# Performance work log

Measured on AMD Instinct MI355X. Metric: run time of the kernel, lower is better.

The kernel has to match this reference:

```python
import jax, jax.numpy as jnp
import numpy as np

B, N, M, LDIM, RDIM, AGG = 4, 512, 512, 512, 512, 256


def setup_inputs() -> dict:
    key = jax.random.key(0)
    ks = jax.random.split(key, 7)
    data = jax.random.normal(ks[0], (B, N, LDIM), dtype=jnp.float32)
    crit = jax.random.normal(ks[1], (B, M, RDIM), dtype=jnp.float32)
    Wl = jax.random.normal(ks[2], (LDIM, AGG), dtype=jnp.float32) / np.sqrt(LDIM)
    bl = jax.random.normal(ks[3], (AGG,), dtype=jnp.float32) * 0.01
    Wr = jax.random.normal(ks[4], (RDIM, AGG), dtype=jnp.float32) / np.sqrt(RDIM)
    br = jax.random.normal(ks[5], (AGG,), dtype=jnp.float32) * 0.01
    agg = jax.random.uniform(ks[6], (AGG,), dtype=jnp.float32, minval=-0.01, maxval=0.01)
    return {"data": data, "crit": crit, "Wl": Wl, "bl": bl, "Wr": Wr, "br": br, "agg": agg}


def reference(data, crit, Wl, bl, Wr, br, agg):
    # linear projections
    datalin = jnp.einsum('bnl,la->bna', data, Wl) + bl   # [B,N,A]
    critlin = jnp.einsum('bmr,ra->bma', crit, Wr) + br   # [B,M,A]
    # broadcast add -> tanh -> reduce with agg vector: [B,N,M]
    linsum = jnp.tanh(datalin[:, :, None, :] + critlin[:, None, :, :])  # [B,N,M,A]
    dists = jnp.einsum('bnma,a->bnm', linsum, agg)
    return dists
```

## Files before the change

### kernel.cpp

```cpp
#include <hip/hip_runtime.h>


#define A_DIM 256
#define K_DIM 512
#define NROWS 2048

typedef unsigned short ushort;
typedef __attribute__((ext_vector_type(4))) unsigned short us4;
typedef __attribute__((ext_vector_type(8))) unsigned short us8;
typedef __attribute__((ext_vector_type(8))) short short8;
typedef __attribute__((ext_vector_type(4))) float f32x4;
typedef __attribute__((ext_vector_type(2))) float f32x2;

__device__ inline ushort f2bf(float x) {
    union { float f; unsigned u; } v; v.f = x;
    unsigned r = v.u + 0x7FFFu + ((v.u >> 16) & 1u);
    return (ushort)(r >> 16);
}
__device__ inline float bf2f(ushort h) {
    union { unsigned u; float f; } v; v.u = ((unsigned)h) << 16; return v.f;
}
__device__ inline unsigned pack2bf(float lo, float hi) {
    return (unsigned)f2bf(lo) | ((unsigned)f2bf(hi) << 16);
}
__device__ inline f32x2 fma2(f32x2 a, f32x2 b, f32x2 c) {
    return __builtin_elementwise_fma(a, b, c);
}

__global__ __launch_bounds__(256) void transpose_w_kernel(
    const float* __restrict__ Wl, const float* __restrict__ Wr,
    ushort* __restrict__ wt)
{
    __shared__ float tile[64][68];
    const int t   = threadIdx.x;
    const int bid = blockIdx.x;
    const int at  = bid & 3;
    const int kt  = (bid >> 2) & 7;
    const int src = bid >> 5;
    const int a0 = at * 64, k0 = kt * 64;
    const float* W = src ? Wr : Wl;
    ushort* out = wt + (size_t)src * (A_DIM * K_DIM);

    const int c4 = (t & 15) * 4;
    const int kr = t >> 4;
#pragma unroll
    for (int r = 0; r < 4; r++) {
        const int k = kr + r * 16;
        *(float4*)&tile[k][c4] = *(const float4*)(W + (size_t)(k0 + k) * A_DIM + a0 + c4);
    }
    __syncthreads();
    const int aL  = t & 63;
    const int ks0 = (t >> 6) * 16;
#pragma unroll
    for (int g = 0; g < 4; g++) {
        us4 o;
#pragma unroll
        for (int i = 0; i < 4; i++) o[i] = f2bf(tile[ks0 + g * 4 + i][aL]);
        __builtin_nontemporal_store(o, (us4*)(out + (size_t)(a0 + aL) * K_DIM + k0 + ks0 + g * 4));
    }
}

__global__ __launch_bounds__(256) void proj_mfma_kernel(
    const float* __restrict__ data, const float* __restrict__ crit,
    const float* __restrict__ bl, const float* __restrict__ br,
    const ushort* __restrict__ wt, ushort* __restrict__ eplanes)
{
    __shared__ ushort Ws[64][264];

    const int t   = threadIdx.x;
    const int bid = blockIdx.x;
    const int ct  = bid & 3;
    const int rt  = bid >> 2;
    const int src = rt >> 6;
    const int lr0 = (rt & 63) * 32;
    const int c0  = ct * 64;

    const float* X    = src ? crit : data;
    const float* bias = src ? br : bl;
    const ushort* Wt  = wt + (size_t)src * (A_DIM * K_DIM);
    ushort* E = eplanes + (size_t)src * ((size_t)A_DIM * NROWS);

    const int lane = t & 63;
    const int wid  = t >> 6;
    const int wm   = wid >> 1, wn = wid & 1;
    const int quad = lane >> 4, l16 = lane & 15;

    const float* xrow = X + (size_t)(lr0 + wm * 16 + l16) * K_DIM + quad * 8;
    const int aloc0 = wn * 32 + l16;

    f32x4 acc0 = {0.f, 0.f, 0.f, 0.f}, acc1 = {0.f, 0.f, 0.f, 0.f};

    float4 pa = *(const float4*)(xrow);
    float4 pb = *(const float4*)(xrow + 4);

    for (int kc = 0; kc < 2; kc++) {
        __syncthreads();
        {
            const int a  = t & 63;
            const int ks = (t >> 6) * 64;
            const ushort* s = Wt + (size_t)(c0 + a) * K_DIM + kc * 256 + ks;
#pragma unroll
            for (int i = 0; i < 8; i++)
                *(us8*)&Ws[a][ks + i * 8] = *(const us8*)(s + i * 8);
        }
        __syncthreads();

#pragma unroll
        for (int ls = 0; ls < 8; ls++) {
            const int s = kc * 8 + ls;
            float4 ca = pa, cb = pb;
            if (s < 15) {
                pa = *(const float4*)(xrow + (s + 1) * 32);
                pb = *(const float4*)(xrow + (s + 1) * 32 + 4);
            }
            union { short8 s8; unsigned u[4]; } af;
            af.u[0] = pack2bf(ca.x, ca.y);
            af.u[1] = pack2bf(ca.z, ca.w);
            af.u[2] = pack2bf(cb.x, cb.y);
            af.u[3] = pack2bf(cb.z, cb.w);
            short8 b0 = *(const short8*)&Ws[aloc0     ][ls * 32 + quad * 8];
            short8 b1 = *(const short8*)&Ws[aloc0 + 16][ls * 32 + quad * 8];
            acc0 = __builtin_amdgcn_mfma_f32_16x16x32_bf16(af.s8, b0, acc0, 0, 0, 0);
            acc1 = __builtin_amdgcn_mfma_f32_16x16x32_bf16(af.s8, b1, acc1, 0, 0, 0);
        }
    }

    const float c2 = 2.8853900817779268f;
    const int a_col0 = c0 + wn * 32 + l16;
    const int a_col1 = a_col0 + 16;
    const int row0   = lr0 + wm * 16 + quad * 4;
    const float bv0 = bias[a_col0], bv1 = bias[a_col1];
    us4 e0, e1;
#pragma unroll
    for (int i = 0; i < 4; i++) {
        float v0 = (acc0[i] + bv0) * c2;
        float v1 = (acc1[i] + bv1) * c2;
        v0 = fminf(fmaxf(v0, -15.f), 15.f);
        v1 = fminf(fmaxf(v1, -15.f), 15.f);
        e0[i] = f2bf(__builtin_amdgcn_exp2f(v0));
        e1[i] = f2bf(__builtin_amdgcn_exp2f(v1));
    }
    __builtin_nontemporal_store(e0, (us4*)(E + (size_t)a_col0 * NROWS + row0));
    __builtin_nontemporal_store(e1, (us4*)(E + (size_t)a_col1 * NROWS + row0));
}

__global__ __launch_bounds__(512) void tanh_reduce_kernel(
    const ushort* __restrict__ eplanes, const float* __restrict__ agg,
    float* __restrict__ out)
{
    __shared__ __align__(16) float et [2][64][68];
    __shared__ __align__(16) float ect[2][64][68];
    __shared__ __align__(16) float aggs[256];

    const int t  = threadIdx.x;
    const int h  = t >> 8;
    const int u  = t & 255;
    const int m0 = blockIdx.x * 64;
    const int n0 = blockIdx.y * 64;
    const int b  = blockIdx.z;

    const size_t PLANE = (size_t)A_DIM * NROWS;
    const ushort* Ed = eplanes;
    const ushort* Ec = eplanes + PLANE;
    const int row_n = b * 512 + n0;
    const int row_m = b * 512 + m0;

    const int tx = u & 15;
    const int ty = u >> 4;

    if (t < 256) aggs[t] = 2.0f * agg[t];

    f32x2 acc2[4][2];
#pragma unroll
    for (int i = 0; i < 4; i++) { acc2[i][0] = (f32x2)0.f; acc2[i][1] = (f32x2)0.f; }
    float sagg = 0.f;

    const int aL = u >> 2;
    const int qd = u & 3;

    float (*eth)[68]  = et[h];
    float (*ecth)[68] = ect[h];

    us4 pn[4], pm[4];
#pragma unroll
    for (int r = 0; r < 4; r++) {
        const size_t base = (size_t)(h * 128 + aL) * NROWS;
        pn[r] = *(const us4*)(Ed + base + row_n + qd * 16 + r * 4);
        pm[r] = *(const us4*)(Ec + base + row_m + qd * 16 + r * 4);
    }

    for (int ch = 0; ch < 2; ch++) {
        __syncthreads();
#pragma unroll
        for (int r = 0; r < 4; r++) {
            float4 ev, cv;
            ev.x = bf2f(pn[r][0]); ev.y = bf2f(pn[r][1]);
            ev.z = bf2f(pn[r][2]); ev.w = bf2f(pn[r][3]);
            cv.x = bf2f(pm[r][0]); cv.y = bf2f(pm[r][1]);
            cv.z = bf2f(pm[r][2]); cv.w = bf2f(pm[r][3]);
            *(float4*)&eth [aL][qd * 16 + r * 4] = ev;
            *(float4*)&ecth[aL][qd * 16 + r * 4] = cv;
        }
        __syncthreads();
        if (ch == 0) {
            const size_t base = (size_t)(h * 128 + 64 + aL) * NROWS;
#pragma unroll
            for (int r = 0; r < 4; r++) {
                pn[r] = *(const us4*)(Ed + base + row_n + qd * 16 + r * 4);
                pm[r] = *(const us4*)(Ec + base + row_m + qd * 16 + r * 4);
            }
        }

        for (int qg = 0; qg < 16; qg++) {
            const float4 ag = *(const float4*)&aggs[h * 128 + ch * 64 + qg * 4];
            sagg += (ag.x + ag.y) + (ag.z + ag.w);
            float  en[4][4];
            f32x2  fm[4][2];
#pragma unroll
            for (int v = 0; v < 4; v++) {
                float4 e4 = *(const float4*)&eth [qg * 4 + v][ty * 4];
                float4 f4 = *(const float4*)&ecth[qg * 4 + v][tx * 4];
                en[v][0] = e4.x; en[v][1] = e4.y; en[v][2] = e4.z; en[v][3] = e4.w;
                fm[v][0] = f32x2{f4.x, f4.y};
                fm[v][1] = f32x2{f4.z, f4.w};
            }
#pragma unroll
            for (int i = 0; i < 4; i++)
#pragma unroll
                for (int jp = 0; jp < 2; jp++) {
                    const f32x2 one = (f32x2)1.f;
                    f32x2 q0 = fma2((f32x2)en[0][i], fm[0][jp], one);
                    f32x2 q1 = fma2((f32x2)en[1][i], fm[1][jp], one);
                    f32x2 q2 = fma2((f32x2)en[2][i], fm[2][jp], one);
                    f32x2 q3 = fma2((f32x2)en[3][i], fm[3][jp], one);
                    f32x2 q01 = q0 * q1, q23 = q2 * q3;
                    f32x2 n01 = fma2((f32x2)ag.x, q1, (f32x2)ag.y * q0);
                    f32x2 n23 = fma2((f32x2)ag.z, q3, (f32x2)ag.w * q2);
                    f32x2 N   = fma2(n01, q23, n23 * q01);
                    f32x2 D   = q01 * q23;
                    f32x2 r;
                    r.x = __builtin_amdgcn_rcpf(D.x);
                    r.y = __builtin_amdgcn_rcpf(D.y);
                    acc2[i][jp] = fma2(N, r, acc2[i][jp]);
                }
        }
    }

    const float base = 0.5f * sagg;
    float* xb = (float*)ect;
    __syncthreads();
    if (h == 1) {
#pragma unroll
        for (int i = 0; i < 4; i++)
#pragma unroll
            for (int jp = 0; jp < 2; jp++) {
                xb[u * 17 + i * 4 + jp * 2 + 0] = base - acc2[i][jp].x;
                xb[u * 17 + i * 4 + jp * 2 + 1] = base - acc2[i][jp].y;
            }
    }
    __syncthreads();
    if (h == 0) {
#pragma unroll
        for (int i = 0; i < 4; i++) {
            f32x4 v;
            v.x = (base - acc2[i][0].x) + xb[u * 17 + i * 4 + 0];
            v.y = (base - acc2[i][0].y) + xb[u * 17 + i * 4 + 1];
            v.z = (base - acc2[i][1].x) + xb[u * 17 + i * 4 + 2];
            v.w = (base - acc2[i][1].y) + xb[u * 17 + i * 4 + 3];
            __builtin_nontemporal_store(v,
                (f32x4*)(out + ((size_t)(b * 512 + n0 + ty * 4 + i) * 512) + m0 + tx * 4));
        }
    }
}

extern "C" void kernel_launch(void* const* d_in, const int* in_sizes, int n_in,
                              void* d_out, int out_size, void* d_ws, size_t ws_size,
                              hipStream_t stream) {
    const float* data = (const float*)d_in[0];
    const float* crit = (const float*)d_in[1];
    const float* Wl   = (const float*)d_in[2];
    const float* bl   = (const float*)d_in[3];
    const float* Wr   = (const float*)d_in[4];
    const float* br   = (const float*)d_in[5];
    const float* agg  = (const float*)d_in[6];
    float* out = (float*)d_out;

    ushort* eplanes = (ushort*)d_ws;
    ushort* wt      = eplanes + 2 * (size_t)A_DIM * NROWS;

    transpose_w_kernel<<<dim3(64), 256, 0, stream>>>(Wl, Wr, wt);

    proj_mfma_kernel<<<dim3(512), 256, 0, stream>>>(data, crit, bl, br, wt, eplanes);

    tanh_reduce_kernel<<<dim3(8, 8, 4), 512, 0, stream>>>(eplanes, agg, out);
}
```

Baseline: 107.8 us.

## Split tanh reduction across four thread groups and single-stage projection weight load

The tanh-reduce kernel now runs 1024 threads per block, with four groups each owning a 64-wide slice of the aggregation dimension. This removes the two-chunk sequential loop, and the four partial results are combined through shared memory. The projection kernel loads the whole 512-wide weight slice into LDS in one stage, prefetches inputs two steps ahead, and reorders block indices so that blocks sharing a weight column tile launch together. The costs are more LDS per block (about 140KB in the reduce kernel), fewer resident blocks per CU, and a larger cross-group reduction at the end.

```diff
diff --git a/kernel.cpp b/kernel.cpp
--- a/kernel.cpp
+++ b/kernel.cpp
@@ -65,12 +65,12 @@
     const float* __restrict__ bl, const float* __restrict__ br,
     const ushort* __restrict__ wt, ushort* __restrict__ eplanes)
 {
-    __shared__ ushort Ws[64][264];
+    __shared__ ushort Ws[64][520];
 
     const int t   = threadIdx.x;
     const int bid = blockIdx.x;
-    const int ct  = bid & 3;
-    const int rt  = bid >> 2;
+    const int ct  = bid >> 7;
+    const int rt  = bid & 127;
     const int src = rt >> 6;
     const int lr0 = (rt & 63) * 32;
     const int c0  = ct * 64;
@@ -90,39 +90,39 @@
 
     f32x4 acc0 = {0.f, 0.f, 0.f, 0.f}, acc1 = {0.f, 0.f, 0.f, 0.f};
 
-    float4 pa = *(const float4*)(xrow);
-    float4 pb = *(const float4*)(xrow + 4);
-
-    for (int kc = 0; kc < 2; kc++) {
-        __syncthreads();
-        {
-            const int a  = t & 63;
-            const int ks = (t >> 6) * 64;
-            const ushort* s = Wt + (size_t)(c0 + a) * K_DIM + kc * 256 + ks;
-#pragma unroll
-            for (int i = 0; i < 8; i++)
-                *(us8*)&Ws[a][ks + i * 8] = *(const us8*)(s + i * 8);
-        }
-        __syncthreads();
-
-#pragma unroll
-        for (int ls = 0; ls < 8; ls++) {
-            const int s = kc * 8 + ls;
-            float4 ca = pa, cb = pb;
-            if (s < 15) {
-                pa = *(const float4*)(xrow + (s + 1) * 32);
-                pb = *(const float4*)(xrow + (s + 1) * 32 + 4);
-            }
-            union { short8 s8; unsigned u[4]; } af;
-            af.u[0] = pack2bf(ca.x, ca.y);
-            af.u[1] = pack2bf(ca.z, ca.w);
-            af.u[2] = pack2bf(cb.x, cb.y);
-            af.u[3] = pack2bf(cb.z, cb.w);
-            short8 b0 = *(const short8*)&Ws[aloc0     ][ls * 32 + quad * 8];
-            short8 b1 = *(const short8*)&Ws[aloc0 + 16][ls * 32 + quad * 8];
-            acc0 = __builtin_amdgcn_mfma_f32_16x16x32_bf16(af.s8, b0, acc0, 0, 0, 0);
-            acc1 = __builtin_amdgcn_mfma_f32_16x16x32_bf16(af.s8, b1, acc1, 0, 0, 0);
-        }
+    {
+        const int a  = t & 63;
+        const int ks = (t >> 6) * 128;
+        const ushort* s = Wt + (size_t)(c0 + a) * K_DIM + ks;
+#pragma unroll
+        for (int i = 0; i < 16; i++)
+            *(us8*)&Ws[a][ks + i * 8] = *(const us8*)(s + i * 8);
+    }
+
+    float4 pa0 = *(const float4*)(xrow);
+    float4 pb0 = *(const float4*)(xrow + 4);
+    float4 pa1 = *(const float4*)(xrow + 32);
+    float4 pb1 = *(const float4*)(xrow + 36);
+
+    __syncthreads();
+
+#pragma unroll
+    for (int s = 0; s < 16; s++) {
+        float4 ca = pa0, cb = pb0;
+        pa0 = pa1; pb0 = pb1;
+        if (s < 14) {
+            pa1 = *(const float4*)(xrow + (s + 2) * 32);
+            pb1 = *(const float4*)(xrow + (s + 2) * 32 + 4);
+        }
+        union { short8 s8; unsigned u[4]; } af;
+        af.u[0] = pack2bf(ca.x, ca.y);
+        af.u[1] = pack2bf(ca.z, ca.w);
+        af.u[2] = pack2bf(cb.x, cb.y);
+        af.u[3] = pack2bf(cb.z, cb.w);
+        short8 b0 = *(const short8*)&Ws[aloc0     ][s * 32 + quad * 8];
+        short8 b1 = *(const short8*)&Ws[aloc0 + 16][s * 32 + quad * 8];
+        acc0 = __builtin_amdgcn_mfma_f32_16x16x32_bf16(af.s8, b0, acc0, 0, 0, 0);
+        acc1 = __builtin_amdgcn_mfma_f32_16x16x32_bf16(af.s8, b1, acc1, 0, 0, 0);
     }
 
     const float c2 = 2.8853900817779268f;
@@ -144,12 +144,12 @@
     __builtin_nontemporal_store(e1, (us4*)(E + (size_t)a_col1 * NROWS + row0));
 }
 
-__global__ __launch_bounds__(512) void tanh_reduce_kernel(
+__global__ __launch_bounds__(1024) void tanh_reduce_kernel(
     const ushort* __restrict__ eplanes, const float* __restrict__ agg,
     float* __restrict__ out)
 {
-    __shared__ __align__(16) float et [2][64][68];
-    __shared__ __align__(16) float ect[2][64][68];
+    __shared__ __align__(16) float et [4][64][68];
+    __shared__ __align__(16) float ect[4][64][68];
     __shared__ __align__(16) float aggs[256];
 
     const int t  = threadIdx.x;
@@ -181,16 +181,14 @@
     float (*eth)[68]  = et[h];
     float (*ecth)[68] = ect[h];
 
-    us4 pn[4], pm[4];
-#pragma unroll
-    for (int r = 0; r < 4; r++) {
-        const size_t base = (size_t)(h * 128 + aL) * NROWS;
-        pn[r] = *(const us4*)(Ed + base + row_n + qd * 16 + r * 4);
-        pm[r] = *(const us4*)(Ec + base + row_m + qd * 16 + r * 4);
-    }
-
-    for (int ch = 0; ch < 2; ch++) {
-        __syncthreads();
+    {
+        const size_t base = (size_t)(h * 64 + aL) * NROWS;
+        us4 pn[4], pm[4];
+#pragma unroll
+        for (int r = 0; r < 4; r++) {
+            pn[r] = *(const us4*)(Ed + base + row_n + qd * 16 + r * 4);
+            pm[r] = *(const us4*)(Ec + base + row_m + qd * 16 + r * 4);
+        }
 #pragma unroll
         for (int r = 0; r < 4; r++) {
             float4 ev, cv;
@@ -201,72 +199,68 @@
             *(float4*)&eth [aL][qd * 16 + r * 4] = ev;
             *(float4*)&ecth[aL][qd * 16 + r * 4] = cv;
         }
-        __syncthreads();
-        if (ch == 0) {
-            const size_t base = (size_t)(h * 128 + 64 + aL) * NROWS;
-#pragma unroll
-            for (int r = 0; r < 4; r++) {
-                pn[r] = *(const us4*)(Ed + base + row_n + qd * 16 + r * 4);
-                pm[r] = *(const us4*)(Ec + base + row_m + qd * 16 + r * 4);
+    }
+    __syncthreads();
+
+    for (int qg = 0; qg < 16; qg++) {
+        const float4 ag = *(const float4*)&aggs[h * 64 + qg * 4];
+        sagg += (ag.x + ag.y) + (ag.z + ag.w);
+        float  en[4][4];
+        f32x2  fm[4][2];
+#pragma unroll
+        for (int v = 0; v < 4; v++) {
+            float4 e4 = *(const float4*)&eth [qg * 4 + v][ty * 4];
+            float4 f4 = *(const float4*)&ecth[qg * 4 + v][tx * 4];
+            en[v][0] = e4.x; en[v][1] = e4.y; en[v][2] = e4.z; en[v][3] = e4.w;
+            fm[v][0] = f32x2{f4.x, f4.y};
+            fm[v][1] = f32x2{f4.z, f4.w};
+        }
+#pragma unroll
+        for (int i = 0; i < 4; i++)
+#pragma unroll
+            for (int jp = 0; jp < 2; jp++) {
+                const f32x2 one = (f32x2)1.f;
+                f32x2 q0 = fma2((f32x2)en[0][i], fm[0][jp], one);
+                f32x2 q1 = fma2((f32x2)en[1][i], fm[1][jp], one);
+                f32x2 q2 = fma2((f32x2)en[2][i], fm[2][jp], one);
+                f32x2 q3 = fma2((f32x2)en[3][i], fm[3][jp], one);
+                f32x2 q01 = q0 * q1, q23 = q2 * q3;
+                f32x2 n01 = fma2((f32x2)ag.x, q1, (f32x2)ag.y * q0);
+                f32x2 n23 = fma2((f32x2)ag.z, q3, (f32x2)ag.w * q2);
+                f32x2 N   = fma2(n01, q23, n23 * q01);
+                f32x2 D   = q01 * q23;
+                f32x2 r;
+                r.x = __builtin_amdgcn_rcpf(D.x);
+                r.y = __builtin_amdgcn_rcpf(D.y);
+                acc2[i][jp] = fma2(N, r, acc2[i][jp]);
             }
-        }
-
-        for (int qg = 0; qg < 16; qg++) {
-            const float4 ag = *(const float4*)&aggs[h * 128 + ch * 64 + qg * 4];
-            sagg += (ag.x + ag.y) + (ag.z + ag.w);
-            float  en[4][4];
-            f32x2  fm[4][2];
-#pragma unroll
-            for (int v = 0; v < 4; v++) {
-                float4 e4 = *(const float4*)&eth [qg * 4 + v][ty * 4];
-                float4 f4 = *(const float4*)&ecth[qg * 4 + v][tx * 4];
-                en[v][0] = e4.x; en[v][1] = e4.y; en[v][2] = e4.z; en[v][3] = e4.w;
-                fm[v][0] = f32x2{f4.x, f4.y};
-                fm[v][1] = f32x2{f4.z, f4.w};
-            }
-#pragma unroll
-            for (int i = 0; i < 4; i++)
-#pragma unroll
-                for (int jp = 0; jp < 2; jp++) {
-                    const f32x2 one = (f32x2)1.f;
-                    f32x2 q0 = fma2((f32x2)en[0][i], fm[0][jp], one);
-                    f32x2 q1 = fma2((f32x2)en[1][i], fm[1][jp], one);
-                    f32x2 q2 = fma2((f32x2)en[2][i], fm[2][jp], one);
-                    f32x2 q3 = fma2((f32x2)en[3][i], fm[3][jp], one);
-                    f32x2 q01 = q0 * q1, q23 = q2 * q3;
-                    f32x2 n01 = fma2((f32x2)ag.x, q1, (f32x2)ag.y * q0);
-                    f32x2 n23 = fma2((f32x2)ag.z, q3, (f32x2)ag.w * q2);
-                    f32x2 N   = fma2(n01, q23, n23 * q01);
-                    f32x2 D   = q01 * q23;
-                    f32x2 r;
-                    r.x = __builtin_amdgcn_rcpf(D.x);
-                    r.y = __builtin_amdgcn_rcpf(D.y);
-                    acc2[i][jp] = fma2(N, r, acc2[i][jp]);
-                }
-        }
     }
 
     const float base = 0.5f * sagg;
     float* xb = (float*)ect;
     __syncthreads();
-    if (h == 1) {
+    if (h != 0) {
+        float* w = xb + ((size_t)(h - 1) * 256 + u) * 17;
 #pragma unroll
         for (int i = 0; i < 4; i++)
 #pragma unroll
             for (int jp = 0; jp < 2; jp++) {
-                xb[u * 17 + i * 4 + jp * 2 + 0] = base - acc2[i][jp].x;
-                xb[u * 17 + i * 4 + jp * 2 + 1] = base - acc2[i][jp].y;
+                w[i * 4 + jp * 2 + 0] = base - acc2[i][jp].x;
+                w[i * 4 + jp * 2 + 1] = base - acc2[i][jp].y;
             }
     }
     __syncthreads();
     if (h == 0) {
+        const float* x1 = xb + (size_t)u * 17;
+        const float* x2 = xb + ((size_t)256 + u) * 17;
+        const float* x3 = xb + ((size_t)512 + u) * 17;
 #pragma unroll
         for (int i = 0; i < 4; i++) {
             f32x4 v;
-            v.x = (base - acc2[i][0].x) + xb[u * 17 + i * 4 + 0];
-            v.y = (base - acc2[i][0].y) + xb[u * 17 + i * 4 + 1];
-            v.z = (base - acc2[i][1].x) + xb[u * 17 + i * 4 + 2];
-            v.w = (base - acc2[i][1].y) + xb[u * 17 + i * 4 + 3];
+            v.x = ((base - acc2[i][0].x) + x1[i * 4 + 0]) + (x2[i * 4 + 0] + x3[i * 4 + 0]);
+            v.y = ((base - acc2[i][0].y) + x1[i * 4 + 1]) + (x2[i * 4 + 1] + x3[i * 4 + 1]);
+            v.z = ((base - acc2[i][1].x) + x1[i * 4 + 2]) + (x2[i * 4 + 2] + x3[i * 4 + 2]);
+            v.w = ((base - acc2[i][1].y) + x1[i * 4 + 3]) + (x2[i * 4 + 3] + x3[i * 4 + 3]);
             __builtin_nontemporal_store(v,
                 (f32x4*)(out + ((size_t)(b * 512 + n0 + ty * 4 + i) * 512) + m0 + tx * 4));
         }
@@ -292,5 +286,5 @@
 
     proj_mfma_kernel<<<dim3(512), 256, 0, stream>>>(data, crit, bl, br, wt, eplanes);
 
-    tanh_reduce_kernel<<<dim3(8, 8, 4), 512, 0, stream>>>(eplanes, agg, out);
-}
+    tanh_reduce_kernel<<<dim3(8, 8, 4), 1024, 0, stream>>>(eplanes, agg, out);
+}
```

Result: no change. 107.2 us (-0.5%).
